# Performance work log

Measured on AMD Instinct MI355X. Metric: run time of the kernel, lower is better.

The kernel has to match this reference:

```python
import jax, jax.numpy as jnp
import numpy as np

EPS = 1e-7
INF = 1e8
NUM_CLASSES = 80
SOFT_CENTER_RADIUS = 3.0
TOPK = 13
IOU_WEIGHT = 3.0
ALPHA = 1.0
BETA = 6.0
IMG = 640.0


def pairwise_iou(b1, b2):
    # b1: (B,N,4), b2: (B,M,4) in xyxy -> (B,N,M) IoU (mmdet BboxOverlaps2D, eps=1e-6)
    a1 = (b1[..., 2] - b1[..., 0]) * (b1[..., 3] - b1[..., 1])
    a2 = (b2[..., 2] - b2[..., 0]) * (b2[..., 3] - b2[..., 1])
    lt = jnp.maximum(b1[:, :, None, :2], b2[:, None, :, :2])
    rb = jnp.minimum(b1[:, :, None, 2:], b2[:, None, :, 2:])
    wh = jnp.clip(rb - lt, 0.0)
    inter = wh[..., 0] * wh[..., 1]
    union = a1[:, :, None] + a2[:, None, :] - inter
    return inter / jnp.maximum(union, 1e-6)


def _forward(pred_bboxes, pred_scores, priors, gt_labels, gt_bboxes, pad_bbox_flag):
    B, P, _ = pred_bboxes.shape
    G = gt_bboxes.shape[1]
    dt = pred_bboxes.dtype
    labels = gt_labels[..., 0]            # (B,G) int
    pad = pad_bbox_flag[..., 0]           # (B,G) float
    prior_xy = priors[:, :2]              # (P,2)
    strides = priors[:, 2]                # (P,)

    # ---- inside-gt test (find_inside_points, box_dim=4): (B,P,G) bool
    lt_ = prior_xy[None, :, None, :] - gt_bboxes[:, None, :, :2]
    rb_ = gt_bboxes[:, None, :, 2:] - prior_xy[None, :, None, :]
    is_in_gts = jnp.minimum(lt_.min(-1), rb_.min(-1)) > 0        # (B,P,G)
    is_in_gts_f = is_in_gts.astype(dt) * pad[:, None, :]         # masked by pad flag
    valid_mask = is_in_gts_f.sum(-1) > 0                          # (B,P)

    # ---- get_pos_mask (TaskAligned metric top-k) -> fg_mask_pre_prior
    overlaps = pairwise_iou(gt_bboxes, pred_bboxes)               # (B,G,P)
    scores_sig = jax.nn.sigmoid(pred_scores)                      # (B,P,C)
    scores_g = jnp.take_along_axis(scores_sig.transpose(0, 2, 1), labels[:, :, None], axis=1)  # (B,G,P)
    align = (scores_g ** ALPHA) * (overlaps ** BETA)              # (B,G,P)
    in_gts_gp = is_in_gts.transpose(0, 2, 1).astype(dt)           # (B,G,P)
    metrics = align * in_gts_gp
    _, topk_idxs = jax.lax.top_k(metrics, TOPK)                   # (B,G,TOPK)
    bb = jnp.arange(B)[:, None, None]
    gg = jnp.arange(G)[None, :, None]
    cnt = jnp.zeros((B, G, P), dt).at[bb, gg, topk_idxs].add(1.0)
    cnt = cnt * pad[:, :, None]
    is_in_topk = jnp.where(cnt > 1, 0.0, cnt)
    pos_mask = is_in_topk * in_gts_gp * pad[:, :, None]           # (B,G,P)
    # select_highest_overlaps: resolve priors matched to >1 gt via max IoU
    fg_pre = pos_mask.sum(1)                                      # (B,P)
    max_gt = overlaps.argmax(1)                                   # (B,P)
    is_max = (jnp.arange(G)[None, None, :] == max_gt[:, :, None]).astype(dt)  # (B,P,G)
    pos_mask = jnp.where((fg_pre > 1)[:, None, :], is_max.transpose(0, 2, 1), pos_mask)
    fg_mask_pre_prior = pos_mask.sum(1) > 0                       # (B,P) bool

    # ---- soft center prior
    gt_center = (gt_bboxes[..., :2] + gt_bboxes[..., 2:]) / 2.0   # (B,G,2)
    dist = jnp.sqrt(((prior_xy[None, :, None, :] - gt_center[:, None, :, :]) ** 2).sum(-1)) \
           / strides[None, :, None]                               # (B,P,G)
    dist = dist * valid_mask[..., None]
    soft_center_prior = jnp.power(10.0, dist - SOFT_CENTER_RADIUS)

    # ---- IoU cost
    pairwise_ious = pairwise_iou(pred_bboxes, gt_bboxes)          # (B,P,G)
    iou_cost = -jnp.log(pairwise_ious + EPS) * IOU_WEIGHT

    # ---- soft classification cost (QFL-style)
    logits = jnp.take_along_axis(pred_scores.transpose(0, 2, 1), labels[:, :, None], axis=1)
    logits = logits.transpose(0, 2, 1)                            # (B,P,G)
    scale = pairwise_ious - jax.nn.sigmoid(logits)
    bce = jnp.logaddexp(0.0, logits) - logits * pairwise_ious     # BCEWithLogits(logits, ious)
    cls_cost = bce * scale ** 2

    cost = cls_cost + iou_cost + soft_center_prior
    cost = jnp.where(valid_mask[..., None], cost, INF)            # (B,P,G)

    # ---- dynamic-k matching
    topk_ious, _ = jax.lax.top_k(pairwise_ious.transpose(0, 2, 1), TOPK)  # (B,G,TOPK)
    dynamic_ks = jnp.maximum(topk_ious.sum(-1).astype(jnp.int32), 1)      # (B,G)
    num_gts = pad.sum(-1).astype(jnp.int32)                                # (B,)
    sorted_idx = jnp.argsort(cost, axis=1)                                 # (B,P,G)
    ranks = jnp.arange(P)[None, :, None]
    gt_valid = jnp.arange(G)[None, :] < num_gts[:, None]                   # (B,G)
    sel = (ranks < dynamic_ks[:, None, :]) & gt_valid[:, None, :]          # (B,P,G), in sorted order
    bb2 = jnp.arange(B)[:, None, None]
    gg2 = jnp.arange(G)[None, None, :]
    matching = jnp.zeros((B, P, G), dt).at[bb2, sorted_idx, gg2].set(sel.astype(dt))
    multi = matching.sum(-1) > 1                                           # (B,P)
    argmin = cost.argmin(-1)                                               # (B,P)
    onehot_min = (jnp.arange(G)[None, None, :] == argmin[:, :, None]).astype(dt)
    matching = jnp.where(multi[..., None], onehot_min, matching)
    fg = matching.sum(-1) > 0                                              # (B,P)
    matched_ious = (matching * pairwise_ious).sum(-1)                      # (B,P)
    matched_gt_inds = matching.argmax(-1)                                  # (B,P)

    # ---- dense outputs (torch scatters into full-size tensors; same values here)
    assigned_labels = jnp.where(fg, jnp.take_along_axis(labels, matched_gt_inds, axis=1), NUM_CLASSES)
    assigned_labels_weights = jnp.ones((B, P), dt)
    assigned_bboxes = jnp.where(fg[..., None],
                                jnp.take_along_axis(gt_bboxes, matched_gt_inds[..., None].repeat(4, -1), axis=1),
                                0.0)
    assign_metrics = jnp.where(fg, matched_ious, 0.0)
    return assigned_labels, assigned_labels_weights, assigned_bboxes, assign_metrics, fg_mask_pre_prior


def setup_inputs() -> dict:
    key = jax.random.key(0)
    ks = jax.random.split(key, 6)
    B, G, C = 16, 100, 80
    # priors: anchor-free grid for 640x640, strides (8,16,32) -> P = 8400
    grids = []
    for s in (8, 16, 32):
        n = 640 // s
        xs = (np.arange(n, dtype=np.float32) + 0.5) * s
        yy, xx = np.meshgrid(xs, xs, indexing='ij')
        g = np.stack([xx.ravel(), yy.ravel(),
                      np.full(n * n, s, np.float32), np.full(n * n, s, np.float32)], -1)
        grids.append(g)
    priors = jnp.asarray(np.concatenate(grids, 0), jnp.float32)  # (8400, 4)
    P = priors.shape[0]

    def rand_boxes(k, shape):
        kc, kw = jax.random.split(k)
        cxy = jax.random.uniform(kc, shape + (2,), minval=0.0, maxval=IMG)
        wh = jax.random.uniform(kw, shape + (2,), minval=8.0, maxval=256.0)
        lt = jnp.clip(cxy - wh / 2, 0.0, IMG)
        rb = jnp.clip(cxy + wh / 2, 0.0, IMG)
        return jnp.concatenate([lt, rb], -1)

    pred_bboxes = rand_boxes(ks[0], (B, P))
    pred_scores = jax.random.normal(ks[1], (B, P, C), jnp.float32) * 2.0 - 2.0
    gt_bboxes = rand_boxes(ks[2], (B, G))
    gt_labels = jax.random.randint(ks[3], (B, G, 1), 0, C)
    n_valid = jax.random.randint(ks[4], (B,), 1, G + 1)
    pad_bbox_flag = (jnp.arange(G)[None, :] < n_valid[:, None]).astype(jnp.float32)[..., None]
    return {"pred_bboxes": pred_bboxes, "pred_scores": pred_scores, "priors": priors,
            "gt_labels": gt_labels, "gt_bboxes": gt_bboxes, "pad_bbox_flag": pad_bbox_flag}


def reference(pred_bboxes, pred_scores, priors, gt_labels, gt_bboxes, pad_bbox_flag):
    return _forward(pred_bboxes, pred_scores, priors, gt_labels, gt_bboxes, pad_bbox_flag)
```

## Files before the change

kernel.cpp:

```cpp
#include <hip/hip_runtime.h>
#include <cstdint>
#include <climits>
#include <cstddef>

#define TK 13
#define MAXG 128
#define CAP 192
#define NW 4
#define MCAP 24576
#define MAXCH 160
#define MBX 8

__device__ __forceinline__ float iou_fn(const float4 pb, const float4 gb){
  float pa = (pb.z - pb.x) * (pb.w - pb.y);
  float ga = (gb.z - gb.x) * (gb.w - gb.y);
  float ltx = fmaxf(pb.x, gb.x), lty = fmaxf(pb.y, gb.y);
  float rbx = fminf(pb.z, gb.z), rby = fminf(pb.w, gb.w);
  float w = fmaxf(rbx - ltx, 0.0f), h = fmaxf(rby - lty, 0.0f);
  float inter = w * h;
  float uni = pa + ga - inter;
  return inter / fmaxf(uni, 1e-6f);
}

__device__ __forceinline__ float sigmoid_f(float x){ return 1.0f / (1.0f + expf(-x)); }

__device__ __forceinline__ float cost_full(float iou, float s, float dist){
  float sig = sigmoid_f(s);
  float iouc = -logf(iou + 1e-7f) * 3.0f;
  float scale = iou - sig;
  float bce = fmaxf(s, 0.0f) + log1pf(expf(-fabsf(s))) - s * iou;
  float cls = bce * scale * scale;
  float soft = powf(10.0f, dist - 3.0f);
  return cls + iouc + soft;
}

__device__ __forceinline__ void bfly_max_u64(unsigned long long &v, int &l){
  #pragma unroll
  for (int off = 32; off >= 1; off >>= 1){
    unsigned long long ov = __shfl_xor(v, off);
    int ol = __shfl_xor(l, off);
    if (ov > v){ v = ov; l = ol; }
  }
}

__device__ __forceinline__ unsigned long long squeeze13(unsigned long long* buf, int& cnt, int lane){
  unsigned long long e0 = (lane < cnt) ? buf[lane] : 0ull;
  unsigned long long e1 = (lane + 64 < cnt) ? buf[lane + 64] : 0ull;
  unsigned long long e2 = (lane + 128 < cnt) ? buf[lane + 128] : 0ull;
  if (e0 < e2){ unsigned long long t = e0; e0 = e2; e2 = t; }
  if (e0 < e1){ unsigned long long t = e0; e0 = e1; e1 = t; }
  if (e1 < e2){ unsigned long long t = e1; e1 = e2; e2 = t; }
  unsigned long long T = 0;
  for (int r = 0; r < TK; ++r){
    unsigned long long m = e0; int l = lane;
    bfly_max_u64(m, l);
    if (lane == 0) buf[r] = m;
    T = m;
    if (lane == l){ e0 = e1; e1 = e2; e2 = 0ull; }
  }
  cnt = TK;
  return T;
}

__global__ __launch_bounds__(256) void k_valid(
    const float4* __restrict__ priors, const float4* __restrict__ pred_bboxes,
    const float4* __restrict__ gtb, const float* __restrict__ pad,
    unsigned long long* __restrict__ vmask, unsigned int* __restrict__ acc,
    unsigned int* __restrict__ mcnt,
    float4* __restrict__ predAB, float4* __restrict__ prAB, float* __restrict__ strC,
    int P, int G, int nCh)
{
  int b = blockIdx.y;
  int p = blockIdx.x * 256 + threadIdx.x;
  if (b == 0 && p == 0) *mcnt = 0u;
  __shared__ float4 sg[MAXG];
  __shared__ float sp[MAXG];
  for (int i = threadIdx.x; i < G; i += 256){ sg[i] = gtb[b*G + i]; sp[i] = pad[b*G + i]; }
  __syncthreads();
  int lane = threadIdx.x & 63;
  int ch = p >> 6;
  bool inb = p < P;
  float4 pr = inb ? priors[p] : make_float4(0,0,0,0);
  float4 pb = inb ? pred_bboxes[(size_t)b*P + p] : make_float4(0,0,0,0);
  bool v = false;
  if (inb){
    #pragma unroll 4
    for (int g = 0; g < G; ++g){
      float4 gb = sg[g];
      bool ig = (pr.x > gb.x) && (pr.y > gb.y) && (gb.z > pr.x) && (gb.w > pr.y);
      v = v || (ig && sp[g] > 0.5f);
    }
    acc[(size_t)b * P + p] = 0u;
  }
  unsigned long long m = __ballot(v);
  if (lane == 0 && ch < nCh) vmask[(size_t)b * nCh + ch] = m;
  float inf = __builtin_inff();
  float x1 = inb ? pb.x : inf,  y1 = inb ? pb.y : inf;
  float x2 = inb ? pb.z : -inf, y2 = inb ? pb.w : -inf;
  float px1 = inb ? pr.x : inf,  py1 = inb ? pr.y : inf;
  float px2 = inb ? pr.x : -inf, py2 = inb ? pr.y : -inf;
  #pragma unroll
  for (int off = 32; off >= 1; off >>= 1){
    x1 = fminf(x1, __shfl_xor(x1, off));  y1 = fminf(y1, __shfl_xor(y1, off));
    x2 = fmaxf(x2, __shfl_xor(x2, off));  y2 = fmaxf(y2, __shfl_xor(y2, off));
    px1 = fminf(px1, __shfl_xor(px1, off)); py1 = fminf(py1, __shfl_xor(py1, off));
    px2 = fmaxf(px2, __shfl_xor(px2, off)); py2 = fmaxf(py2, __shfl_xor(py2, off));
  }
  if (lane == 0 && ch < nCh){
    predAB[(size_t)b * nCh + ch] = make_float4(x1, y1, x2, y2);
    if (b == 0){ prAB[ch] = make_float4(px1, py1, px2, py2); strC[ch] = pr.z; }
  }
}

__global__ __launch_bounds__(256) void k_scan(
    const float4* __restrict__ pred_bboxes, const float* __restrict__ pred_scores,
    const float4* __restrict__ priors, const int* __restrict__ gt_labels,
    const float4* __restrict__ gtbb, const float* __restrict__ pad,
    const unsigned long long* __restrict__ vmask,
    const float4* __restrict__ predAB, const float4* __restrict__ prAB,
    const float* __restrict__ strC,
    unsigned int* __restrict__ acc, unsigned int* __restrict__ mcnt,
    unsigned int* __restrict__ mlist,
    int P, int G, int C, int nCh)
{
  int bg = blockIdx.x;
  if (pad[bg] <= 0.5f) return;
  int b = bg / G;
  int g = bg - b * G;
  int tid = threadIdx.x;
  int lane = tid & 63;
  int wv = tid >> 6;
  float4 gb = gtbb[bg];
  int lbl = gt_labels[bg];
  float gcx = (gb.x + gb.z) * 0.5f, gcy = (gb.y + gb.w) * 0.5f;
  size_t bP = (size_t)b * P;
  const unsigned long long* vmb = vmask + (size_t)b * nCh;
  const float4* pAB = predAB + (size_t)b * nCh;
  const unsigned B1E8 = __float_as_uint(1e8f);

  __shared__ unsigned long long bufM[NW*CAP], bufC[NW*CAP], bufI[NW*CAP];
  __shared__ uint2 sgeo[MAXCH];
  __shared__ unsigned long long svm[MAXCH];
  __shared__ unsigned int shwC, shwM, shwI;
  if (tid == 0){ shwC = 0xFFFFFFFFu; shwM = 0u; shwI = 0u; }
  for (int ch = tid; ch < nCh; ch += 256){
    float4 pA = pAB[ch];
    float4 rA = prAB[ch];
    float strc = strC[ch];
    bool geoI = !(pA.x < gb.z && pA.z > gb.x && pA.y < gb.w && pA.w > gb.y);
    bool geoM = !(rA.z > gb.x && rA.x < gb.z && rA.w > gb.y && rA.y < gb.w);
    float dxr = fmaxf(0.0f, fmaxf(rA.x - gcx, gcx - rA.z));
    float dyr = fmaxf(0.0f, fmaxf(rA.y - gcy, gcy - rA.w));
    float drr = sqrtf(dxr*dxr + dyr*dyr) / strc;
    sgeo[ch] = make_uint2((geoI ? 1u : 0u) | (geoM ? 2u : 0u), __float_as_uint(drr));
    svm[ch] = vmb[ch];
  }
  __syncthreads();
  unsigned long long* bM = bufM + wv*CAP;
  unsigned long long* bC = bufC + wv*CAP;
  unsigned long long* bI = bufI + wv*CAP;

  int cntM = 0, cntC = 0, cntI = 0;
  int zM = 0, zC = 0;
  unsigned long long Tm = 0ull, Tc = 0ull;
  unsigned long long Ti = 0x00000000FFFFFFFFull;
  unsigned cbits = 0xFFFFFFFFu, mBbits = 0u, iBb = 0u;
  float thr = 1e30f, mB = 0.0f;
  unsigned long long laneLT = (1ull << lane) - 1ull;

  int c0 = wv;
  int pf = c0 * 64 + lane;
  bool inb = (c0 < nCh) && (pf < P);
  float4 pb = inb ? pred_bboxes[bP + pf] : make_float4(0,0,0,0);
  for (int c = c0; c < nCh; c += NW){
    int cn = c + NW;
    int pn = cn * 64 + lane;
    bool inbn = (cn < nCh) && (pn < P);
    float4 pbn = make_float4(0,0,0,0);
    if (inbn) pbn = pred_bboxes[bP + pn];
    { unsigned sC = shwC; if (sC < cbits){ cbits = sC;
        thr = 3.0f + log10f(__uint_as_float(cbits) * 1.00002f + 1e-6f); } }
    { unsigned sM = shwM; if (sM > mBbits){ mBbits = sM; mB = __uint_as_float(sM); } }
    { unsigned sI = shwI; if (sI > iBb) iBb = sI; }
    uint2 ge = sgeo[c];
    bool geoI = (ge.x & 1u) != 0u;
    bool geoM = (ge.x & 2u) != 0u;
    float drr = __uint_as_float(ge.y);
    bool poolM = (zM >= TK) || (mBbits > 0u);
    bool poolC = (zC >= TK) || (cbits < B1E8);
    bool skipMt = geoM && poolM;
    bool skipCt = (drr > thr) && poolC;
    if (!(geoI && skipMt && skipCt)){
      int p = c * 64 + lane;
      float iou = iou_fn(pb, gb);
      unsigned long long keyI = ((unsigned long long)__float_as_uint(iou) << 32) | (unsigned)p;
      bool candI = inb && (keyI > Ti) && !((unsigned)(keyI >> 32) < iBb);
      if (cntI > CAP - 64){
        Ti = squeeze13(bI, cntI, lane);
        unsigned ib = (unsigned)(Ti >> 32);
        if (ib > iBb) iBb = ib;
        if (lane == 0 && ib) atomicMax(&shwI, ib);
        candI = candI && (keyI > Ti) && !((unsigned)(keyI >> 32) < iBb);
      }
      { unsigned long long mk = __ballot(candI);
        if (mk){ int off = cntI + __popcll(mk & laneLT); if (candI) bI[off] = keyI; cntI += __popcll(mk); } }
      if (!(skipMt && skipCt)){
        float4 pr = inb ? priors[p] : make_float4(0,0,0,0);
        bool vb = inb && (((svm[c] >> lane) & 1ull) != 0ull);
        bool ig = inb && (pr.x > gb.x) && (pr.y > gb.y) && (gb.z > pr.x) && (gb.w > pr.y);
        bool pos = ig && (iou > 0.0f);
        float i2 = iou * iou;
        float bnd = (i2 * i2) * i2 * 1.000002f;
        bool needm = pos && !(bnd < mB);
        float dist = 0.0f; bool needc = false;
        if (vb){
          float dx = pr.x - gcx, dy = pr.y - gcy;
          dist = sqrtf(dx*dx + dy*dy) / pr.z;
          needc = !(dist > thr);
        }
        float sc = 0.0f;
        if (needm || needc) sc = pred_scores[(bP + p) * C + lbl];
        unsigned long long keyM = 0;
        if (__ballot(needm)){
          float met = sigmoid_f(sc) * powf(iou, 6.0f);
          if (needm)
            keyM = ((unsigned long long)__float_as_uint(met) << 32)
                 | (unsigned)~(unsigned)((p << 1) | 1);
        }
        if (zM < TK && inb && !pos)
          keyM = (unsigned long long)(unsigned)~(unsigned)((p << 1) | (ig ? 1 : 0));
        bool candM = (keyM != 0ull) && (keyM > Tm) && !((unsigned)(keyM >> 32) < mBbits);
        unsigned long long keyC = 0;
        if (zC < TK && inb && !vb)
          keyC = ~(((unsigned long long)__float_as_uint(1e8f) << 32) | (unsigned)p);
        if (__ballot(needc)){
          float cst = cost_full(iou, sc, dist);
          if (needc)
            keyC = ~(((unsigned long long)__float_as_uint(cst) << 32) | (unsigned)p);
        }
        bool candC = (keyC != 0ull) && (keyC > Tc) && !((unsigned)((~keyC) >> 32) > cbits);
        if (cntM > CAP - 64){
          Tm = squeeze13(bM, cntM, lane);
          unsigned tb = (unsigned)(Tm >> 32);
          if (tb > mBbits){ mBbits = tb; mB = __uint_as_float(tb); }
          if (lane == 0 && tb) atomicMax(&shwM, tb);
          candM = candM && (keyM > Tm) && !((unsigned)(keyM >> 32) < mBbits);
        }
        { unsigned long long mk = __ballot(candM);
          if (mk){
            int off = cntM + __popcll(mk & laneLT);
            if (candM) bM[off] = keyM;
            cntM += __popcll(mk);
            unsigned long long zk = __ballot(candM && !pos);
            zM += __popcll(zk);
          } }
        if (cntC > CAP - 64){
          Tc = squeeze13(bC, cntC, lane);
          unsigned cb = (unsigned)((~Tc) >> 32);
          if (cb < cbits){ cbits = cb;
            thr = 3.0f + log10f(__uint_as_float(cbits) * 1.00002f + 1e-6f); }
          if (lane == 0) atomicMin(&shwC, cb);
          candC = candC && (keyC > Tc) && !((unsigned)((~keyC) >> 32) > cbits);
        }
        { unsigned long long mk = __ballot(candC);
          if (mk){
            int off = cntC + __popcll(mk & laneLT);
            if (candC) bC[off] = keyC;
            cntC += __popcll(mk);
            unsigned long long zk = __ballot(candC && !vb);
            zC += __popcll(zk);
          } }
      }
    }
    pb = pbn; inb = inbn;
  }

  squeeze13(bI, cntI, lane);
  squeeze13(bM, cntM, lane);
  squeeze13(bC, cntC, lane);
  __syncthreads();
  if (wv != 0) return;

  int w13 = lane / TK, r13 = lane - w13 * TK;
  int kd;
  {
    unsigned long long e = (lane < NW*TK) ? bufI[w13*CAP + r13] : 0ull;
    float ksum = 0.0f;
    for (int r = 0; r < TK; ++r){
      unsigned long long m = e; int l = lane;
      bfly_max_u64(m, l);
      ksum += __uint_as_float((unsigned)(m >> 32));
      if (lane == l) e = 0ull;
    }
    kd = (int)ksum; if (kd < 1) kd = 1;
  }
  {
    unsigned long long e = (lane < NW*TK) ? bufM[w13*CAP + r13] : 0ull;
    for (int r = 0; r < TK; ++r){
      unsigned long long m = e; int l = lane;
      bfly_max_u64(m, l);
      if (m == 0ull) break;
      if (lane == 0){
        unsigned ix = ~(unsigned)(m & 0xFFFFFFFFull);
        if (ix & 1u) atomicOr(&acc[bP + (ix >> 1)], 2u);
      }
      if (lane == l) e = 0ull;
    }
  }
  {
    unsigned long long e = (lane < NW*TK) ? bufC[w13*CAP + r13] : 0ull;
    for (int r = 0; r < kd; ++r){
      unsigned long long m = e; int l = lane;
      bfly_max_u64(m, l);
      if (m == 0ull) break;
      if (lane == 0){
        unsigned pp = (unsigned)((~m) & 0xFFFFFFFFull);
        unsigned old = atomicAdd(&acc[bP + pp], (1u << 17) | ((unsigned)g << 2));
        if ((old >> 17) == 1u){
          unsigned mi = atomicAdd(mcnt, 1u);
          if (mi < MCAP) mlist[mi] = (unsigned)(bP + pp);
        }
      }
      if (lane == l) e = 0ull;
    }
  }
}

__global__ __launch_bounds__(256) void k_fm(
    const float4* __restrict__ pred_bboxes, const float* __restrict__ pred_scores,
    const float4* __restrict__ priors, const int* __restrict__ gt_labels,
    const float4* __restrict__ gtb, const unsigned long long* __restrict__ vmask,
    const unsigned int* __restrict__ acc,
    const unsigned int* __restrict__ mcnt, const unsigned int* __restrict__ mlist,
    float* __restrict__ out, int B, int P, int G, int C, int nCh, int nDecX)
{
  size_t BP = (size_t)B * P;
  if ((int)blockIdx.x >= nDecX){
    unsigned n = *mcnt; if (n > MCAP) n = MCAP;
    int lane = threadIdx.x & 63;
    int widx = ((int)blockIdx.y * MBX + ((int)blockIdx.x - nDecX)) * (blockDim.x >> 6)
             + ((int)threadIdx.x >> 6);
    int nw = gridDim.y * MBX * (blockDim.x >> 6);
    for (unsigned i = widx; i < n; i += nw){
      unsigned o = mlist[i];
      int b = o / P;
      int p = o - b * P;
      float4 pb = pred_bboxes[o];
      bool vld = (vmask[(size_t)b * nCh + (p >> 6)] >> (p & 63)) & 1ull;
      int mg = 0;
      if (vld){
        float4 pr = priors[p];
        const float* srow = pred_scores + (size_t)o * C;
        unsigned long long best = 0xFFFFFFFFFFFFFFFFull;
        for (int g0 = lane; g0 < G; g0 += 64){
          float4 gbx = gtb[b*G + g0];
          float iou = iou_fn(pb, gbx);
          float s = srow[gt_labels[b*G + g0]];
          float gcx = (gbx.x + gbx.z) * 0.5f, gcy = (gbx.y + gbx.w) * 0.5f;
          float dx = pr.x - gcx, dy = pr.y - gcy;
          float dist = sqrtf(dx*dx + dy*dy) / pr.z;
          float cc = cost_full(iou, s, dist);
          unsigned long long k = ((unsigned long long)__float_as_uint(cc) << 32) | (unsigned)g0;
          if (k < best) best = k;
        }
        #pragma unroll
        for (int off = 32; off >= 1; off >>= 1){
          unsigned long long ov = __shfl_xor(best, off);
          if (ov < best) best = ov;
        }
        mg = (int)(best & 0xFFFFFFFFull);
      }
      if (lane == 0){
        float4 gbx = gtb[b*G + mg];
        out[o] = (float)gt_labels[b*G + mg];
        ((float4*)(out + 2*BP))[o] = gbx;
        out[6*BP + o] = iou_fn(pb, gbx);
      }
    }
    return;
  }
  int b = blockIdx.y;
  int p = blockIdx.x * 256 + threadIdx.x;
  __shared__ float4 sg[MAXG];
  __shared__ int sl[MAXG];
  for (int i = threadIdx.x; i < G; i += 256){
    sg[i] = gtb[b*G + i]; sl[i] = gt_labels[b*G + i];
  }
  __syncthreads();
  if (p >= P) return;
  size_t o = (size_t)b * P + p;
  unsigned int w = acc[o];
  int cnt = (int)(w >> 17);
  out[BP + o] = 1.0f;
  out[7*BP + o] = ((w >> 1) & 1u) ? 1.0f : 0.0f;
  if (cnt > 1) return;
  bool fg = cnt > 0;
  int mg = fg ? (int)((w >> 2) & 0x7FFFu) : 0;
  float4 pb = pred_bboxes[o];
  out[o] = fg ? (float)sl[mg] : 80.0f;
  float4 ob = fg ? sg[mg] : make_float4(0.f, 0.f, 0.f, 0.f);
  ((float4*)(out + 2*BP))[o] = ob;
  out[6*BP + o] = fg ? iou_fn(pb, sg[mg]) : 0.0f;
}

extern "C" void kernel_launch(void* const* d_in, const int* in_sizes, int n_in,
                              void* d_out, int out_size, void* d_ws, size_t ws_size,
                              hipStream_t stream)
{
  const float4* pred_bboxes = (const float4*)d_in[0];
  const float*  pred_scores = (const float*)d_in[1];
  const float4* priors      = (const float4*)d_in[2];
  const int*    gt_labels   = (const int*)d_in[3];
  const float4* gt_bboxes   = (const float4*)d_in[4];
  const float*  pad         = (const float*)d_in[5];
  int P = in_sizes[2] / 4;
  int B = in_sizes[0] / (P * 4);
  int C = in_sizes[1] / (B * P);
  int G = in_sizes[4] / (B * 4);
  int BG = B * G;
  int nCh = (P + 63) >> 6;

  uint8_t* ws = (uint8_t*)d_ws;
  size_t off = 0;
  unsigned long long* vmask = (unsigned long long*)(ws + off); off += (size_t)B * nCh * 8;
  unsigned int* acc = (unsigned int*)(ws + off);               off += (size_t)B * P * 4;
  off = (off + 15) & ~(size_t)15;
  unsigned int* mcnt = (unsigned int*)(ws + off);              off += 16;
  unsigned int* mlist = (unsigned int*)(ws + off);             off += (size_t)MCAP * 4;
  off = (off + 15) & ~(size_t)15;
  float4* predAB = (float4*)(ws + off);                        off += (size_t)B * nCh * 16;
  float4* prAB = (float4*)(ws + off);                          off += (size_t)nCh * 16;
  float* strC = (float*)(ws + off);                            off += (size_t)nCh * 4;
  float* out = (float*)d_out;

  int nDecX = (P + 255) / 256;
  dim3 gridA(nDecX, B);
  dim3 gridF(nDecX + MBX, B);
  k_valid<<<gridA, 256, 0, stream>>>(priors, pred_bboxes, gt_bboxes, pad,
                                     vmask, acc, mcnt, predAB, prAB, strC, P, G, nCh);
  k_scan<<<BG, NW*64, 0, stream>>>(pred_bboxes, pred_scores, priors, gt_labels,
                                   gt_bboxes, pad, vmask, predAB, prAB, strC,
                                   acc, mcnt, mlist, P, G, C, nCh);
  k_fm<<<gridF, 256, 0, stream>>>(pred_bboxes, pred_scores, priors, gt_labels,
                                  gt_bboxes, vmask, acc, mcnt, mlist, out,
                                  B, P, G, C, nCh, nDecX);
}
```

Baseline: 262.6 us.

## Split top-13 IoU sum into separate split-chunk kernel feeding scan kernel

Moves the per-GT top-13 IoU search (used for the dynamic-k sum) out of the scan kernel into a new kernel launched over (BG, 8 splits). Each wave keeps a register-resident sorted top-13 per lane and merges the results into a per-split list in workspace. The scan kernel now only skips chunks on the metric and cost criteria and reduces the 8x13 partial values with a float butterfly. This drops the IoU candidate buffer, its atomics and the software prefetch from the scan loop. The cost is an extra launch, a second read of pred_bboxes, and the loss of the combined geometric skip that the old IoU test allowed.

```diff
diff --git a/kernel.cpp b/kernel.cpp
--- a/kernel.cpp
+++ b/kernel.cpp
@@ -7,6 +7,7 @@
 #define MAXG 128
 #define CAP 192
 #define NW 4
+#define SI 8
 #define MCAP 24576
 #define MAXCH 160
 #define MBX 8
@@ -112,13 +113,62 @@
   }
 }
 
+__global__ __launch_bounds__(64) void k_iou(
+    const float4* __restrict__ pred_bboxes, const float4* __restrict__ gtbb,
+    const float* __restrict__ pad, const float4* __restrict__ predAB,
+    float* __restrict__ wsI, int P, int G, int nCh)
+{
+  int bg = blockIdx.x;
+  int s  = blockIdx.y;
+  if (pad[bg] <= 0.5f) return;
+  int b = bg / G;
+  int lane = threadIdx.x;
+  float4 gb = gtbb[bg];
+  size_t bP = (size_t)b * P;
+  const float4* pAB = predAB + (size_t)b * nCh;
+  float ivl[TK];
+  #pragma unroll
+  for (int j = 0; j < TK; ++j) ivl[j] = 0.0f;
+  for (int c = s; c < nCh; c += SI){
+    float4 pA = pAB[c];
+    bool ov = (pA.x < gb.z) && (pA.z > gb.x) && (pA.y < gb.w) && (pA.w > gb.y);
+    if (!ov) continue;
+    int p = c * 64 + lane;
+    if (p >= P) continue;
+    float4 pb = pred_bboxes[bP + p];
+    float iou = iou_fn(pb, gb);
+    if (iou > ivl[TK-1]){
+      float v = iou;
+      #pragma unroll
+      for (int j = 0; j < TK; ++j){ if (v > ivl[j]){ float t = ivl[j]; ivl[j] = v; v = t; } }
+    }
+  }
+  __shared__ float slst[64 * TK];
+  #pragma unroll
+  for (int j = 0; j < TK; ++j) slst[lane*TK + j] = ivl[j];
+  __syncthreads();
+  int ptr = 0;
+  float h = slst[lane*TK];
+  float* dst = wsI + ((size_t)bg * SI + s) * TK;
+  for (int r = 0; r < TK; ++r){
+    float v = h; int l = lane;
+    #pragma unroll
+    for (int off = 32; off >= 1; off >>= 1){
+      float o2 = __shfl_xor(v, off); int ol = __shfl_xor(l, off);
+      if (o2 > v || (o2 == v && ol < l)){ v = o2; l = ol; }
+    }
+    if (lane == 0) dst[r] = v;
+    if (lane == l){ ptr++; h = (ptr < TK) ? slst[lane*TK + ptr] : -1.0f; }
+  }
+}
+
 __global__ __launch_bounds__(256) void k_scan(
     const float4* __restrict__ pred_bboxes, const float* __restrict__ pred_scores,
     const float4* __restrict__ priors, const int* __restrict__ gt_labels,
     const float4* __restrict__ gtbb, const float* __restrict__ pad,
     const unsigned long long* __restrict__ vmask,
     const float4* __restrict__ predAB, const float4* __restrict__ prAB,
-    const float* __restrict__ strC,
+    const float* __restrict__ strC, const float* __restrict__ wsI,
     unsigned int* __restrict__ acc, unsigned int* __restrict__ mcnt,
     unsigned int* __restrict__ mlist,
     int P, int G, int C, int nCh)
@@ -135,165 +185,141 @@
   float gcx = (gb.x + gb.z) * 0.5f, gcy = (gb.y + gb.w) * 0.5f;
   size_t bP = (size_t)b * P;
   const unsigned long long* vmb = vmask + (size_t)b * nCh;
-  const float4* pAB = predAB + (size_t)b * nCh;
   const unsigned B1E8 = __float_as_uint(1e8f);
 
-  __shared__ unsigned long long bufM[NW*CAP], bufC[NW*CAP], bufI[NW*CAP];
+  __shared__ unsigned long long bufM[NW*CAP], bufC[NW*CAP];
   __shared__ uint2 sgeo[MAXCH];
   __shared__ unsigned long long svm[MAXCH];
-  __shared__ unsigned int shwC, shwM, shwI;
-  if (tid == 0){ shwC = 0xFFFFFFFFu; shwM = 0u; shwI = 0u; }
+  __shared__ unsigned int shwC, shwM;
+  if (tid == 0){ shwC = 0xFFFFFFFFu; shwM = 0u; }
   for (int ch = tid; ch < nCh; ch += 256){
-    float4 pA = pAB[ch];
     float4 rA = prAB[ch];
     float strc = strC[ch];
-    bool geoI = !(pA.x < gb.z && pA.z > gb.x && pA.y < gb.w && pA.w > gb.y);
     bool geoM = !(rA.z > gb.x && rA.x < gb.z && rA.w > gb.y && rA.y < gb.w);
     float dxr = fmaxf(0.0f, fmaxf(rA.x - gcx, gcx - rA.z));
     float dyr = fmaxf(0.0f, fmaxf(rA.y - gcy, gcy - rA.w));
     float drr = sqrtf(dxr*dxr + dyr*dyr) / strc;
-    sgeo[ch] = make_uint2((geoI ? 1u : 0u) | (geoM ? 2u : 0u), __float_as_uint(drr));
+    sgeo[ch] = make_uint2(geoM ? 1u : 0u, __float_as_uint(drr));
     svm[ch] = vmb[ch];
   }
   __syncthreads();
   unsigned long long* bM = bufM + wv*CAP;
   unsigned long long* bC = bufC + wv*CAP;
-  unsigned long long* bI = bufI + wv*CAP;
-
-  int cntM = 0, cntC = 0, cntI = 0;
+
+  int cntM = 0, cntC = 0;
   int zM = 0, zC = 0;
   unsigned long long Tm = 0ull, Tc = 0ull;
-  unsigned long long Ti = 0x00000000FFFFFFFFull;
-  unsigned cbits = 0xFFFFFFFFu, mBbits = 0u, iBb = 0u;
+  unsigned cbits = 0xFFFFFFFFu, mBbits = 0u;
   float thr = 1e30f, mB = 0.0f;
   unsigned long long laneLT = (1ull << lane) - 1ull;
 
-  int c0 = wv;
-  int pf = c0 * 64 + lane;
-  bool inb = (c0 < nCh) && (pf < P);
-  float4 pb = inb ? pred_bboxes[bP + pf] : make_float4(0,0,0,0);
-  for (int c = c0; c < nCh; c += NW){
-    int cn = c + NW;
-    int pn = cn * 64 + lane;
-    bool inbn = (cn < nCh) && (pn < P);
-    float4 pbn = make_float4(0,0,0,0);
-    if (inbn) pbn = pred_bboxes[bP + pn];
+  for (int c = wv; c < nCh; c += NW){
     { unsigned sC = shwC; if (sC < cbits){ cbits = sC;
         thr = 3.0f + log10f(__uint_as_float(cbits) * 1.00002f + 1e-6f); } }
     { unsigned sM = shwM; if (sM > mBbits){ mBbits = sM; mB = __uint_as_float(sM); } }
-    { unsigned sI = shwI; if (sI > iBb) iBb = sI; }
     uint2 ge = sgeo[c];
-    bool geoI = (ge.x & 1u) != 0u;
-    bool geoM = (ge.x & 2u) != 0u;
+    bool geoM = (ge.x & 1u) != 0u;
     float drr = __uint_as_float(ge.y);
     bool poolM = (zM >= TK) || (mBbits > 0u);
     bool poolC = (zC >= TK) || (cbits < B1E8);
     bool skipMt = geoM && poolM;
     bool skipCt = (drr > thr) && poolC;
-    if (!(geoI && skipMt && skipCt)){
-      int p = c * 64 + lane;
-      float iou = iou_fn(pb, gb);
-      unsigned long long keyI = ((unsigned long long)__float_as_uint(iou) << 32) | (unsigned)p;
-      bool candI = inb && (keyI > Ti) && !((unsigned)(keyI >> 32) < iBb);
-      if (cntI > CAP - 64){
-        Ti = squeeze13(bI, cntI, lane);
-        unsigned ib = (unsigned)(Ti >> 32);
-        if (ib > iBb) iBb = ib;
-        if (lane == 0 && ib) atomicMax(&shwI, ib);
-        candI = candI && (keyI > Ti) && !((unsigned)(keyI >> 32) < iBb);
-      }
-      { unsigned long long mk = __ballot(candI);
-        if (mk){ int off = cntI + __popcll(mk & laneLT); if (candI) bI[off] = keyI; cntI += __popcll(mk); } }
-      if (!(skipMt && skipCt)){
-        float4 pr = inb ? priors[p] : make_float4(0,0,0,0);
-        bool vb = inb && (((svm[c] >> lane) & 1ull) != 0ull);
-        bool ig = inb && (pr.x > gb.x) && (pr.y > gb.y) && (gb.z > pr.x) && (gb.w > pr.y);
-        bool pos = ig && (iou > 0.0f);
-        float i2 = iou * iou;
-        float bnd = (i2 * i2) * i2 * 1.000002f;
-        bool needm = pos && !(bnd < mB);
-        float dist = 0.0f; bool needc = false;
-        if (vb){
-          float dx = pr.x - gcx, dy = pr.y - gcy;
-          dist = sqrtf(dx*dx + dy*dy) / pr.z;
-          needc = !(dist > thr);
-        }
-        float sc = 0.0f;
-        if (needm || needc) sc = pred_scores[(bP + p) * C + lbl];
-        unsigned long long keyM = 0;
-        if (__ballot(needm)){
-          float met = sigmoid_f(sc) * powf(iou, 6.0f);
-          if (needm)
-            keyM = ((unsigned long long)__float_as_uint(met) << 32)
-                 | (unsigned)~(unsigned)((p << 1) | 1);
-        }
-        if (zM < TK && inb && !pos)
-          keyM = (unsigned long long)(unsigned)~(unsigned)((p << 1) | (ig ? 1 : 0));
-        bool candM = (keyM != 0ull) && (keyM > Tm) && !((unsigned)(keyM >> 32) < mBbits);
-        unsigned long long keyC = 0;
-        if (zC < TK && inb && !vb)
-          keyC = ~(((unsigned long long)__float_as_uint(1e8f) << 32) | (unsigned)p);
-        if (__ballot(needc)){
-          float cst = cost_full(iou, sc, dist);
-          if (needc)
-            keyC = ~(((unsigned long long)__float_as_uint(cst) << 32) | (unsigned)p);
-        }
-        bool candC = (keyC != 0ull) && (keyC > Tc) && !((unsigned)((~keyC) >> 32) > cbits);
-        if (cntM > CAP - 64){
-          Tm = squeeze13(bM, cntM, lane);
-          unsigned tb = (unsigned)(Tm >> 32);
-          if (tb > mBbits){ mBbits = tb; mB = __uint_as_float(tb); }
-          if (lane == 0 && tb) atomicMax(&shwM, tb);
-          candM = candM && (keyM > Tm) && !((unsigned)(keyM >> 32) < mBbits);
-        }
-        { unsigned long long mk = __ballot(candM);
-          if (mk){
-            int off = cntM + __popcll(mk & laneLT);
-            if (candM) bM[off] = keyM;
-            cntM += __popcll(mk);
-            unsigned long long zk = __ballot(candM && !pos);
-            zM += __popcll(zk);
-          } }
-        if (cntC > CAP - 64){
-          Tc = squeeze13(bC, cntC, lane);
-          unsigned cb = (unsigned)((~Tc) >> 32);
-          if (cb < cbits){ cbits = cb;
-            thr = 3.0f + log10f(__uint_as_float(cbits) * 1.00002f + 1e-6f); }
-          if (lane == 0) atomicMin(&shwC, cb);
-          candC = candC && (keyC > Tc) && !((unsigned)((~keyC) >> 32) > cbits);
-        }
-        { unsigned long long mk = __ballot(candC);
-          if (mk){
-            int off = cntC + __popcll(mk & laneLT);
-            if (candC) bC[off] = keyC;
-            cntC += __popcll(mk);
-            unsigned long long zk = __ballot(candC && !vb);
-            zC += __popcll(zk);
-          } }
-      }
-    }
-    pb = pbn; inb = inbn;
-  }
-
-  squeeze13(bI, cntI, lane);
+    if (skipMt && skipCt) continue;
+    int p = c * 64 + lane;
+    bool inb = p < P;
+    float4 pb = inb ? pred_bboxes[bP + p] : make_float4(0,0,0,0);
+    float iou = iou_fn(pb, gb);
+    float4 pr = inb ? priors[p] : make_float4(0,0,0,0);
+    bool vb = inb && (((svm[c] >> lane) & 1ull) != 0ull);
+    bool ig = inb && (pr.x > gb.x) && (pr.y > gb.y) && (gb.z > pr.x) && (gb.w > pr.y);
+    bool pos = ig && (iou > 0.0f);
+    float i2 = iou * iou;
+    float bnd = (i2 * i2) * i2 * 1.000002f;
+    bool needm = pos && !(bnd < mB);
+    float dist = 0.0f; bool needc = false;
+    if (vb){
+      float dx = pr.x - gcx, dy = pr.y - gcy;
+      dist = sqrtf(dx*dx + dy*dy) / pr.z;
+      needc = !(dist > thr);
+    }
+    float sc = 0.0f;
+    if (needm || needc) sc = pred_scores[(bP + p) * C + lbl];
+    unsigned long long keyM = 0;
+    if (__ballot(needm)){
+      float met = sigmoid_f(sc) * powf(iou, 6.0f);
+      if (needm)
+        keyM = ((unsigned long long)__float_as_uint(met) << 32)
+             | (unsigned)~(unsigned)((p << 1) | 1);
+    }
+    if (zM < TK && inb && !pos)
+      keyM = (unsigned long long)(unsigned)~(unsigned)((p << 1) | (ig ? 1 : 0));
+    bool candM = (keyM != 0ull) && (keyM > Tm) && !((unsigned)(keyM >> 32) < mBbits);
+    unsigned long long keyC = 0;
+    if (zC < TK && inb && !vb)
+      keyC = ~(((unsigned long long)__float_as_uint(1e8f) << 32) | (unsigned)p);
+    if (__ballot(needc)){
+      float cst = cost_full(iou, sc, dist);
+      if (needc)
+        keyC = ~(((unsigned long long)__float_as_uint(cst) << 32) | (unsigned)p);
+    }
+    bool candC = (keyC != 0ull) && (keyC > Tc) && !((unsigned)((~keyC) >> 32) > cbits);
+    if (cntM > CAP - 64){
+      Tm = squeeze13(bM, cntM, lane);
+      unsigned tb = (unsigned)(Tm >> 32);
+      if (tb > mBbits){ mBbits = tb; mB = __uint_as_float(tb); }
+      if (lane == 0 && tb) atomicMax(&shwM, tb);
+      candM = candM && (keyM > Tm) && !((unsigned)(keyM >> 32) < mBbits);
+    }
+    { unsigned long long mk = __ballot(candM);
+      if (mk){
+        int off = cntM + __popcll(mk & laneLT);
+        if (candM) bM[off] = keyM;
+        cntM += __popcll(mk);
+        unsigned long long zk = __ballot(candM && !pos);
+        zM += __popcll(zk);
+      } }
+    if (cntC > CAP - 64){
+      Tc = squeeze13(bC, cntC, lane);
+      unsigned cb = (unsigned)((~Tc) >> 32);
+      if (cb < cbits){ cbits = cb;
+        thr = 3.0f + log10f(__uint_as_float(cbits) * 1.00002f + 1e-6f); }
+      if (lane == 0) atomicMin(&shwC, cb);
+      candC = candC && (keyC > Tc) && !((unsigned)((~keyC) >> 32) > cbits);
+    }
+    { unsigned long long mk = __ballot(candC);
+      if (mk){
+        int off = cntC + __popcll(mk & laneLT);
+        if (candC) bC[off] = keyC;
+        cntC += __popcll(mk);
+        unsigned long long zk = __ballot(candC && !vb);
+        zC += __popcll(zk);
+      } }
+  }
+
   squeeze13(bM, cntM, lane);
   squeeze13(bC, cntC, lane);
   __syncthreads();
   if (wv != 0) return;
 
-  int w13 = lane / TK, r13 = lane - w13 * TK;
   int kd;
   {
-    unsigned long long e = (lane < NW*TK) ? bufI[w13*CAP + r13] : 0ull;
+    const float* wi = wsI + (size_t)bg * (SI*TK);
+    float e0 = (lane < SI*TK) ? wi[lane] : -1.0f;
+    float e1 = (lane + 64 < SI*TK) ? wi[lane + 64] : -1.0f;
     float ksum = 0.0f;
     for (int r = 0; r < TK; ++r){
-      unsigned long long m = e; int l = lane;
-      bfly_max_u64(m, l);
-      ksum += __uint_as_float((unsigned)(m >> 32));
-      if (lane == l) e = 0ull;
+      float m = fmaxf(e0, e1); int l = lane;
+      #pragma unroll
+      for (int off = 32; off >= 1; off >>= 1){
+        float ov = __shfl_xor(m, off); int ol = __shfl_xor(l, off);
+        if (ov > m || (ov == m && ol < l)){ m = ov; l = ol; }
+      }
+      ksum += m;
+      if (lane == l){ if (e0 >= e1) e0 = -1.0f; else e1 = -1.0f; }
     }
     kd = (int)ksum; if (kd < 1) kd = 1;
   }
+  int w13 = lane / TK, r13 = lane - w13 * TK;
   {
     unsigned long long e = (lane < NW*TK) ? bufM[w13*CAP + r13] : 0ull;
     for (int r = 0; r < TK; ++r){
@@ -431,6 +457,8 @@
   float4* predAB = (float4*)(ws + off);                        off += (size_t)B * nCh * 16;
   float4* prAB = (float4*)(ws + off);                          off += (size_t)nCh * 16;
   float* strC = (float*)(ws + off);                            off += (size_t)nCh * 4;
+  off = (off + 15) & ~(size_t)15;
+  float* wsI = (float*)(ws + off);                             off += (size_t)BG * SI * TK * 4;
   float* out = (float*)d_out;
 
   int nDecX = (P + 255) / 256;
@@ -438,8 +466,10 @@
   dim3 gridF(nDecX + MBX, B);
   k_valid<<<gridA, 256, 0, stream>>>(priors, pred_bboxes, gt_bboxes, pad,
                                      vmask, acc, mcnt, predAB, prAB, strC, P, G, nCh);
+  k_iou<<<dim3(BG, SI), 64, 0, stream>>>(pred_bboxes, gt_bboxes, pad, predAB,
+                                         wsI, P, G, nCh);
   k_scan<<<BG, NW*64, 0, stream>>>(pred_bboxes, pred_scores, priors, gt_labels,
-                                   gt_bboxes, pad, vmask, predAB, prAB, strC,
+                                   gt_bboxes, pad, vmask, predAB, prAB, strC, wsI,
                                    acc, mcnt, mlist, P, G, C, nCh);
   k_fm<<<gridF, 256, 0, stream>>>(pred_bboxes, pred_scores, priors, gt_labels,
                                   gt_bboxes, vmask, acc, mcnt, mlist, out,
```

Result: slower. 281.4 us (+7.2%).
